# Optimization experiments

Hardware: AMD Instinct MI355X
Metric: run time of the kernel (lower is better)

The kernel has to match this reference:

```python
import jax, jax.numpy as jnp
import numpy as np

# Batched/grouped formulation of nnmd's per-atom AtomicNN energy evaluation.
# Original: e_nn[s, a] = AtomicNN_a(g[s, a]) in a python double loop.
# Here each atom a has its own MLP (5 -> 64 -> 64 -> 1, tanh hidden activations),
# fused into grouped GEMMs via einsum over the atom axis.

S, A, D = 4096, 1024, 5   # n_structs, n_atoms, input_nodes (descriptors)
H = 64                    # hidden width (hidden_nodes = [64, 64])


def setup_inputs() -> dict:
    key = jax.random.key(0)
    k = jax.random.split(key, 4)
    g = jax.random.normal(k[0], (S, A, D), dtype=jnp.float32)
    W1 = jax.random.normal(k[1], (A, D, H), dtype=jnp.float32)
    b1 = jnp.zeros((A, H), dtype=jnp.float32)
    W2 = jax.random.normal(k[2], (A, H, H), dtype=jnp.float32)
    b2 = jnp.zeros((A, H), dtype=jnp.float32)
    W3 = jax.random.normal(k[3], (A, H, 1), dtype=jnp.float32)
    b3 = jnp.zeros((A, 1), dtype=jnp.float32)
    return {"g": g, "W1": W1, "b1": b1, "W2": W2, "b2": b2, "W3": W3, "b3": b3}


def reference(g, W1, b1, W2, b2, W3, b3):
    # g: [S, A, D]; per-atom weights carry leading A axis -> grouped GEMMs.
    h = jnp.tanh(jnp.einsum('sad,adh->sah', g, W1) + b1)   # [S, A, H]
    h = jnp.tanh(jnp.einsum('sah,ahk->sak', h, W2) + b2)   # [S, A, H]
    e = jnp.einsum('sak,ako->sao', h, W3) + b3             # [S, A, 1]
    return e[..., 0]                                       # e_nn: [S, A]
```

## Files before the change

kernel.cpp:

```cpp
#include <hip/hip_runtime.h>
#include <hip/hip_bf16.h>

typedef __bf16 bf16x8 __attribute__((ext_vector_type(8)));
typedef __bf16 bf16x4 __attribute__((ext_vector_type(4)));
typedef float  f32x4  __attribute__((ext_vector_type(4)));
typedef unsigned short u16;
typedef unsigned int   u32;

#define K2L 2.88539008177792681472f

__device__ inline float tanh_ps(float zs) {
    float E = __builtin_amdgcn_exp2f(zs);
    return fmaf(-2.0f, __builtin_amdgcn_rcpf(E + 1.0f), 1.0f);
}
__device__ inline float tanhK_ps(float zs) {
    float E = __builtin_amdgcn_exp2f(zs);
    return fmaf(-2.0f * K2L, __builtin_amdgcn_rcpf(E + 1.0f), K2L);
}
__device__ inline float bfbits2f(u16 u) {
    u32 v = ((u32)u) << 16;
    return __builtin_bit_cast(float, v);
}

__global__ __launch_bounds__(256, 4)
void atomicnn_kernel(const void* __restrict__ g,  const void* __restrict__ W1,
                     const void* __restrict__ b1, const void* __restrict__ W2,
                     const void* __restrict__ b2, const void* __restrict__ W3,
                     const void* __restrict__ b3, void* __restrict__ out)
{
    constexpr int A = 1024, SROWS = 512;
    constexpr int HS = 72;

    __shared__ __align__(16) __bf16 s_w1[8 * 64];
    __shared__ __align__(16) __bf16 s_w2[64 * 64];
    __shared__ float s_b1f[64], s_b2f[64];
    __shared__ __align__(16) __bf16 s_w3b[64];
    __shared__ __align__(16) __bf16 s_g[SROWS * 8];
    __shared__ __align__(16) __bf16 s_h[4 * 2 * 16 * HS];

    const int tid   = threadIdx.x;
    const int a     = blockIdx.x;
    const int sbase = blockIdx.y * SROWS;
    const int lane  = tid & 63;
    const int wave  = tid >> 6;
    const int sub   = lane & 15;
    const int quad  = lane >> 4;

    int cnt = 0;
    {
        const u16* gp16 = (const u16*)g;
        #pragma unroll
        for (int d = 0; d < 4; ++d) {
            u16 v = gp16[lane * 4 + d];
            u32 e = ((u32)v >> 7) & 0xFF;
            cnt += (int)__popcll(__ballot(e >= 100 && e <= 140));
        }
    }
    const int bfmode = (cnt >= 200) ? 1 : 0;

    if (bfmode) {
        const u16* W2g = (const u16*)W2 + (size_t)a * 4096;
        {
            int p = tid >> 2, c = (tid & 3) * 16;
            int u = (p >> 2) + 16 * (p & 3);
            const uint4* src = (const uint4*)(W2g + u * 64 + c);
            uint4* dst = (uint4*)((u16*)s_w2 + p * 64 + c);
            dst[0] = src[0]; dst[1] = src[1];
        }
        if (tid < 40) {
            ((uint4*)s_w1)[tid] = ((const uint4*)((const u16*)W1 + (size_t)a * 320))[tid];
        } else if (tid < 64) {
            ((uint4*)s_w1)[tid] = make_uint4(0, 0, 0, 0);
        }
        if (tid < 64) {
            s_b1f[tid] = K2L * bfbits2f(((const u16*)b1)[(size_t)a * 64 + tid]);
            s_b2f[tid] = K2L * bfbits2f(((const u16*)b2)[(size_t)a * 64 + tid]);
            s_w3b[tid] = __builtin_bit_cast(__bf16, ((const u16*)W3)[(size_t)a * 64 + tid]);
        }
        for (int i = tid; i < SROWS; i += 256) {
            const u16* gp = (const u16*)g + ((size_t)(sbase + i) * A + a) * 5;
            bf16x8 row = {};
            #pragma unroll
            for (int d = 0; d < 5; ++d) row[d] = (__bf16)(K2L * bfbits2f(gp[d]));
            *(bf16x8*)&s_g[i * 8] = row;
        }
    } else {
        const float* W2f = (const float*)W2 + (size_t)a * 4096;
        for (int i = tid; i < 4096; i += 256) {
            int p = i >> 6, c2 = i & 63;
            int u = (p >> 2) + 16 * (p & 3);
            s_w2[i] = (__bf16)W2f[u * 64 + c2];
        }
        for (int i = tid; i < 512; i += 256)
            s_w1[i] = (i < 320) ? (__bf16)((const float*)W1)[(size_t)a * 320 + i] : (__bf16)0.0f;
        if (tid < 64) {
            s_b1f[tid] = K2L * ((const float*)b1)[(size_t)a * 64 + tid];
            s_b2f[tid] = K2L * ((const float*)b2)[(size_t)a * 64 + tid];
            s_w3b[tid] = (__bf16)((const float*)W3)[(size_t)a * 64 + tid];
        }
        for (int i = tid; i < SROWS; i += 256) {
            const float* gp = (const float*)g + ((size_t)(sbase + i) * A + a) * 5;
            bf16x8 row = {};
            #pragma unroll
            for (int d = 0; d < 5; ++d) row[d] = (__bf16)(K2L * gp[d]);
            *(bf16x8*)&s_g[i * 8] = row;
        }
    }
    __syncthreads();

    bf16x8 bw1[4];
    bf16x8 bw2[2][4];
    bf16x8 bw3[2];
    f32x4 cb1[4], cb2[4], cb3;
    #pragma unroll
    for (int t = 0; t < 4; ++t) {
        const int col = sub + 16 * t;
        float v1 = s_b1f[col], v2 = s_b2f[col];
        cb1[t] = (f32x4){v1, v1, v1, v1};
        cb2[t] = (f32x4){v2, v2, v2, v2};
        #pragma unroll
        for (int j = 0; j < 8; ++j) {
            bw1[t][j]    = (quad == 0) ? s_w1[j * 64 + col] : (__bf16)0.0f;
            bw2[0][t][j] = s_w2[(quad * 8 + j) * 64 + col];
            bw2[1][t][j] = s_w2[(32 + quad * 8 + j) * 64 + col];
        }
    }
    #pragma unroll
    for (int kc = 0; kc < 2; ++kc)
        #pragma unroll
        for (int j = 0; j < 8; ++j) {
            int p = kc * 32 + quad * 8 + j;
            int u = (p >> 2) + 16 * (p & 3);
            bw3[kc][j] = (sub == 0) ? s_w3b[u] : (__bf16)0.0f;
        }
    const float b3f = bfmode ? bfbits2f(((const u16*)b3)[a]) : ((const float*)b3)[a];
    cb3 = (f32x4){b3f, b3f, b3f, b3f};

    __bf16* hping = s_h + wave * (2 * 16 * HS);
    const int rowbase = wave * 128;

    const __bf16* agp = (quad == 0) ? &s_g[(rowbase + sub) * 8] : &s_w1[5 * 64];
    const int aginc = (quad == 0) ? (16 * 8) : 0;

    #pragma unroll 2
    for (int gi = 0; gi < 8; ++gi) {
        const int r0 = rowbase + gi * 16;
        __bf16* hrow = hping + (gi & 1) * (16 * HS);

        if ((gi & 1) == 0)
            asm volatile("" ::: "memory");

        bf16x8 ag = *(const bf16x8*)agp;
        agp += aginc;

        f32x4 acc1[4];
        #pragma unroll
        for (int t = 0; t < 4; ++t)
            acc1[t] = __builtin_amdgcn_mfma_f32_16x16x32_bf16(ag, bw1[t], cb1[t], 0, 0, 0);

        #pragma unroll
        for (int r = 0; r < 4; ++r) {
            bf16x4 hv;
            #pragma unroll
            for (int t = 0; t < 4; ++t) hv[t] = (__bf16)tanhK_ps(acc1[t][r]);
            *(bf16x4*)&hrow[(quad * 4 + r) * HS + 4 * sub] = hv;
        }

        f32x4 acc2[4];
        {
            bf16x8 ah0 = *(const bf16x8*)&hrow[sub * HS + quad * 8];
            #pragma unroll
            for (int t = 0; t < 4; ++t)
                acc2[t] = __builtin_amdgcn_mfma_f32_16x16x32_bf16(ah0, bw2[0][t], cb2[t], 0, 0, 0);
            bf16x8 ah1 = *(const bf16x8*)&hrow[sub * HS + 32 + quad * 8];
            #pragma unroll
            for (int t = 0; t < 4; ++t)
                acc2[t] = __builtin_amdgcn_mfma_f32_16x16x32_bf16(ah1, bw2[1][t], acc2[t], 0, 0, 0);
        }

        #pragma unroll
        for (int r = 0; r < 4; ++r) {
            bf16x4 hv;
            #pragma unroll
            for (int t = 0; t < 4; ++t) hv[t] = (__bf16)tanh_ps(acc2[t][r]);
            *(bf16x4*)&hrow[(quad * 4 + r) * HS + 4 * sub] = hv;
        }

        f32x4 acc3;
        {
            bf16x8 ah0 = *(const bf16x8*)&hrow[sub * HS + quad * 8];
            acc3 = __builtin_amdgcn_mfma_f32_16x16x32_bf16(ah0, bw3[0], cb3, 0, 0, 0);
            bf16x8 ah1 = *(const bf16x8*)&hrow[sub * HS + 32 + quad * 8];
            acc3 = __builtin_amdgcn_mfma_f32_16x16x32_bf16(ah1, bw3[1], acc3, 0, 0, 0);
        }
        if (sub == 0) {
            #pragma unroll
            for (int r = 0; r < 4; ++r) {
                size_t o = (size_t)(sbase + r0 + quad * 4 + r) * A + a;
                if (bfmode) ((u16*)out)[o] = __builtin_bit_cast(u16, (__bf16)acc3[r]);
                else        ((float*)out)[o] = acc3[r];
            }
        }
    }
}

extern "C" void kernel_launch(void* const* d_in, const int* in_sizes, int n_in,
                              void* d_out, int out_size, void* d_ws, size_t ws_size,
                              hipStream_t stream) {
    const void *g = 0, *W1 = 0, *b1 = 0, *W2 = 0, *b2 = 0, *W3 = 0, *b3 = 0;
    const void* trip[3]; int nt = 0;
    for (int i = 0; i < n_in; ++i) {
        int sz = in_sizes[i];
        if      (sz == 20971520) g  = d_in[i];
        else if (sz == 327680)   W1 = d_in[i];
        else if (sz == 4194304)  W2 = d_in[i];
        else if (sz == 1024)     b3 = d_in[i];
        else if (sz == 65536 && nt < 3) trip[nt++] = d_in[i];
    }
    if (nt == 3) {
        bool alpha = (n_in >= 1 && in_sizes[0] == 327680);
        if (alpha) { W3 = trip[0]; b1 = trip[1]; b2 = trip[2]; }
        else       { b1 = trip[0]; b2 = trip[1]; W3 = trip[2]; }
    }
    if (!g || !W1 || !b1 || !W2 || !b2 || !W3 || !b3) {
        g = d_in[0]; W1 = d_in[1]; b1 = d_in[2]; W2 = d_in[3];
        b2 = d_in[4]; W3 = d_in[5]; b3 = d_in[6];
    }

    dim3 grid(1024, 8);
    atomicnn_kernel<<<grid, 256, 0, stream>>>(g, W1, b1, W2, b2, W3, b3, d_out);
}
```

Before: 289.1 us.

## Pack tanh outputs with cheap bf16 rounding, single h buffer, raise occupancy

Replaces the compiler's bf16 conversion with an add-and-perm round that packs two values per 32-bit word, and applies it to the tanh outputs, the g staging and the output stores. Drops the ping-pong hidden buffer for one buffer per wave to cut LDS, and raises the launch-bounds occupancy hint from 4 to 5. Output pointers are now advanced incrementally. The simplified rounding skips round-to-nearest-even tie handling and NaN care. Adding compiler memory barriers after each stage may restrict scheduling overlap.

```diff
diff --git a/kernel.cpp b/kernel.cpp
--- a/kernel.cpp
+++ b/kernel.cpp
@@ -2,41 +2,42 @@
 #include <hip/hip_bf16.h>
 
 typedef __bf16 bf16x8 __attribute__((ext_vector_type(8)));
-typedef __bf16 bf16x4 __attribute__((ext_vector_type(4)));
 typedef float  f32x4  __attribute__((ext_vector_type(4)));
 typedef unsigned short u16;
 typedef unsigned int   u32;
 
 #define K2L 2.88539008177792681472f
 
-__device__ inline float tanh_ps(float zs) {
-    float E = __builtin_amdgcn_exp2f(zs);
-    return fmaf(-2.0f, __builtin_amdgcn_rcpf(E + 1.0f), 1.0f);
-}
-__device__ inline float tanhK_ps(float zs) {
-    float E = __builtin_amdgcn_exp2f(zs);
-    return fmaf(-2.0f * K2L, __builtin_amdgcn_rcpf(E + 1.0f), K2L);
-}
 __device__ inline float bfbits2f(u16 u) {
     u32 v = ((u32)u) << 16;
     return __builtin_bit_cast(float, v);
 }
-
-__global__ __launch_bounds__(256, 4)
+__device__ inline u32 pack_bf16_rn(float a, float b) {
+    u32 ua = __builtin_bit_cast(u32, a) + 0x8000u;
+    u32 ub = __builtin_bit_cast(u32, b) + 0x8000u;
+    return __builtin_amdgcn_perm(ub, ua, 0x07060302);
+}
+__device__ inline u32 tanh2_pack(float z0, float z1, float m, float c) {
+    float r0 = __builtin_amdgcn_rcpf(__builtin_amdgcn_exp2f(z0) + 1.0f);
+    float r1 = __builtin_amdgcn_rcpf(__builtin_amdgcn_exp2f(z1) + 1.0f);
+    return pack_bf16_rn(fmaf(m, r0, c), fmaf(m, r1, c));
+}
+
+__global__ __launch_bounds__(256, 5)
 void atomicnn_kernel(const void* __restrict__ g,  const void* __restrict__ W1,
                      const void* __restrict__ b1, const void* __restrict__ W2,
                      const void* __restrict__ b2, const void* __restrict__ W3,
                      const void* __restrict__ b3, void* __restrict__ out)
 {
     constexpr int A = 1024, SROWS = 512;
-    constexpr int HS = 72;
+    constexpr int HSW = 36;
 
     __shared__ __align__(16) __bf16 s_w1[8 * 64];
     __shared__ __align__(16) __bf16 s_w2[64 * 64];
     __shared__ float s_b1f[64], s_b2f[64];
     __shared__ __align__(16) __bf16 s_w3b[64];
     __shared__ __align__(16) __bf16 s_g[SROWS * 8];
-    __shared__ __align__(16) __bf16 s_h[4 * 2 * 16 * HS];
+    __shared__ __align__(16) u32 s_h[4 * 16 * HSW];
 
     const int tid   = threadIdx.x;
     const int a     = blockIdx.x;
@@ -79,10 +80,15 @@
         }
         for (int i = tid; i < SROWS; i += 256) {
             const u16* gp = (const u16*)g + ((size_t)(sbase + i) * A + a) * 5;
-            bf16x8 row = {};
-            #pragma unroll
-            for (int d = 0; d < 5; ++d) row[d] = (__bf16)(K2L * bfbits2f(gp[d]));
-            *(bf16x8*)&s_g[i * 8] = row;
+            float v0 = K2L * bfbits2f(gp[0]), v1 = K2L * bfbits2f(gp[1]);
+            float v2 = K2L * bfbits2f(gp[2]), v3 = K2L * bfbits2f(gp[3]);
+            float v4 = K2L * bfbits2f(gp[4]);
+            uint4 pk;
+            pk.x = pack_bf16_rn(v0, v1);
+            pk.y = pack_bf16_rn(v2, v3);
+            pk.z = pack_bf16_rn(v4, 0.0f);
+            pk.w = 0;
+            *(uint4*)&s_g[i * 8] = pk;
         }
     } else {
         const float* W2f = (const float*)W2 + (size_t)a * 4096;
@@ -100,10 +106,12 @@
         }
         for (int i = tid; i < SROWS; i += 256) {
             const float* gp = (const float*)g + ((size_t)(sbase + i) * A + a) * 5;
-            bf16x8 row = {};
-            #pragma unroll
-            for (int d = 0; d < 5; ++d) row[d] = (__bf16)(K2L * gp[d]);
-            *(bf16x8*)&s_g[i * 8] = row;
+            uint4 pk;
+            pk.x = pack_bf16_rn(K2L * gp[0], K2L * gp[1]);
+            pk.y = pack_bf16_rn(K2L * gp[2], K2L * gp[3]);
+            pk.z = pack_bf16_rn(K2L * gp[4], 0.0f);
+            pk.w = 0;
+            *(uint4*)&s_g[i * 8] = pk;
         }
     }
     __syncthreads();
@@ -136,19 +144,19 @@
     const float b3f = bfmode ? bfbits2f(((const u16*)b3)[a]) : ((const float*)b3)[a];
     cb3 = (f32x4){b3f, b3f, b3f, b3f};
 
-    __bf16* hping = s_h + wave * (2 * 16 * HS);
+    u32* hw = s_h + wave * (16 * HSW);
+    const __bf16* hr = (const __bf16*)hw;
     const int rowbase = wave * 128;
 
     const __bf16* agp = (quad == 0) ? &s_g[(rowbase + sub) * 8] : &s_w1[5 * 64];
     const int aginc = (quad == 0) ? (16 * 8) : 0;
 
+    u16*   outb = (u16*)out   + (size_t)(sbase + rowbase + quad * 4) * A + a;
+    float* outf = (float*)out + (size_t)(sbase + rowbase + quad * 4) * A + a;
+
     #pragma unroll 2
     for (int gi = 0; gi < 8; ++gi) {
-        const int r0 = rowbase + gi * 16;
-        __bf16* hrow = hping + (gi & 1) * (16 * HS);
-
-        if ((gi & 1) == 0)
-            asm volatile("" ::: "memory");
+        asm volatile("" ::: "memory");
 
         bf16x8 ag = *(const bf16x8*)agp;
         agp += aginc;
@@ -160,47 +168,51 @@
 
         #pragma unroll
         for (int r = 0; r < 4; ++r) {
-            bf16x4 hv;
-            #pragma unroll
-            for (int t = 0; t < 4; ++t) hv[t] = (__bf16)tanhK_ps(acc1[t][r]);
-            *(bf16x4*)&hrow[(quad * 4 + r) * HS + 4 * sub] = hv;
-        }
+            uint2 hv;
+            hv.x = tanh2_pack(acc1[0][r], acc1[1][r], -2.0f * K2L, K2L);
+            hv.y = tanh2_pack(acc1[2][r], acc1[3][r], -2.0f * K2L, K2L);
+            *(uint2*)&hw[(quad * 4 + r) * HSW + 2 * sub] = hv;
+        }
+        asm volatile("" ::: "memory");
 
         f32x4 acc2[4];
         {
-            bf16x8 ah0 = *(const bf16x8*)&hrow[sub * HS + quad * 8];
+            bf16x8 ah0 = *(const bf16x8*)&hr[sub * 2 * HSW + quad * 8];
             #pragma unroll
             for (int t = 0; t < 4; ++t)
                 acc2[t] = __builtin_amdgcn_mfma_f32_16x16x32_bf16(ah0, bw2[0][t], cb2[t], 0, 0, 0);
-            bf16x8 ah1 = *(const bf16x8*)&hrow[sub * HS + 32 + quad * 8];
+            bf16x8 ah1 = *(const bf16x8*)&hr[sub * 2 * HSW + 32 + quad * 8];
             #pragma unroll
             for (int t = 0; t < 4; ++t)
                 acc2[t] = __builtin_amdgcn_mfma_f32_16x16x32_bf16(ah1, bw2[1][t], acc2[t], 0, 0, 0);
         }
+        asm volatile("" ::: "memory");
 
         #pragma unroll
         for (int r = 0; r < 4; ++r) {
-            bf16x4 hv;
-            #pragma unroll
-            for (int t = 0; t < 4; ++t) hv[t] = (__bf16)tanh_ps(acc2[t][r]);
-            *(bf16x4*)&hrow[(quad * 4 + r) * HS + 4 * sub] = hv;
-        }
+            uint2 hv;
+            hv.x = tanh2_pack(acc2[0][r], acc2[1][r], -2.0f, 1.0f);
+            hv.y = tanh2_pack(acc2[2][r], acc2[3][r], -2.0f, 1.0f);
+            *(uint2*)&hw[(quad * 4 + r) * HSW + 2 * sub] = hv;
+        }
+        asm volatile("" ::: "memory");
 
         f32x4 acc3;
         {
-            bf16x8 ah0 = *(const bf16x8*)&hrow[sub * HS + quad * 8];
+            bf16x8 ah0 = *(const bf16x8*)&hr[sub * 2 * HSW + quad * 8];
             acc3 = __builtin_amdgcn_mfma_f32_16x16x32_bf16(ah0, bw3[0], cb3, 0, 0, 0);
-            bf16x8 ah1 = *(const bf16x8*)&hrow[sub * HS + 32 + quad * 8];
+            bf16x8 ah1 = *(const bf16x8*)&hr[sub * 2 * HSW + 32 + quad * 8];
             acc3 = __builtin_amdgcn_mfma_f32_16x16x32_bf16(ah1, bw3[1], acc3, 0, 0, 0);
         }
         if (sub == 0) {
             #pragma unroll
             for (int r = 0; r < 4; ++r) {
-                size_t o = (size_t)(sbase + r0 + quad * 4 + r) * A + a;
-                if (bfmode) ((u16*)out)[o] = __builtin_bit_cast(u16, (__bf16)acc3[r]);
-                else        ((float*)out)[o] = acc3[r];
+                if (bfmode) outb[(size_t)r * A] = (u16)(pack_bf16_rn(acc3[r], 0.0f) & 0xFFFF);
+                else        outf[(size_t)r * A] = acc3[r];
             }
         }
+        outb += (size_t)16 * A;
+        outf += (size_t)16 * A;
     }
 }
 
```

Measured after the change: 740.4 us. 156% more time.
